# Kernel optimization log

Hardware: AMD Instinct MI355X
Metric: run time of the kernel (lower is better)

Reference implementation:

```python
import jax, jax.numpy as jnp
import numpy as np

N = 500_000
E = 16_000_000


def setup_inputs() -> dict:
    key = jax.random.key(0)
    k1, k2, k3, k4, k5 = jax.random.split(key, 5)
    x = jax.random.uniform(k1, (N, 11), dtype=jnp.float32)
    edge_index = jax.random.randint(k2, (2, E), 0, N, dtype=jnp.int32)
    edge_weight = jax.random.uniform(k3, (E,), dtype=jnp.float32)
    W1 = jax.random.normal(k4, (11, 16), dtype=jnp.float32) * 0.3
    b1 = jnp.zeros((16,), jnp.float32)
    W2 = jax.random.normal(k5, (16, 2), dtype=jnp.float32) * 0.3
    b2 = jnp.zeros((2,), jnp.float32)
    return {"x": x, "edge_index": edge_index, "edge_weight": edge_weight,
            "W1": W1, "b1": b1, "W2": W2, "b2": b2}


def gcn_norm(edge_index, edge_weight, n):
    # GCNConv(normalize=True, add_self_loops=True): A_hat = D^-1/2 (A + I) D^-1/2
    self_idx = jnp.arange(n, dtype=edge_index.dtype)
    row = jnp.concatenate([edge_index[0], self_idx])  # source
    col = jnp.concatenate([edge_index[1], self_idx])  # target
    w = jnp.concatenate([edge_weight, jnp.ones((n,), edge_weight.dtype)])
    deg = jax.ops.segment_sum(w, col, num_segments=n)
    dinv = jnp.where(deg > 0, jax.lax.rsqrt(deg), 0.0)
    norm = dinv[row] * w * dinv[col]
    return row, col, norm


def gcn_conv(x, row, col, norm, W, b, n):
    h = x @ W                                   # [N, F_out]
    msg = norm[:, None] * h[row]                # gather + scale, [E+N, F_out]
    out = jax.ops.segment_sum(msg, col, num_segments=n)  # scatter-add
    return out + b


def reference(x, edge_index, edge_weight, W1, b1, W2, b2):
    n = x.shape[0]
    row, col, norm = gcn_norm(edge_index, edge_weight, n)
    h = jax.nn.relu(gcn_conv(x, row, col, norm, W1, b1, n))
    # dropout is identity in eval / deterministic reference
    h = gcn_conv(h, row, col, norm, W2, b2, n)
    return jax.nn.log_softmax(h, axis=1)
```

## Files before the change

kernel.cpp:

```cpp
#include <hip/hip_runtime.h>
#include <math.h>


typedef unsigned long long u64;
typedef unsigned int u32;
typedef _Float16 f16;
typedef __attribute__((ext_vector_type(4))) _Float16 f16x4;

#define BKT    512
#define NBMAX  1024
#define NBLK   256


__global__ __launch_bounds__(256) void k_count(const int* __restrict__ col,
                                               u32* __restrict__ hist_g,
                                               int NB, int E, int CH) {
    __shared__ u32 cnt[NBMAX];
    for (int b = threadIdx.x; b < NB; b += 256) cnt[b] = 0;
    __syncthreads();
    int blk = blockIdx.x;
    int s = blk * CH, e = min(s + CH, E);
    for (int i = s + threadIdx.x; i < e; i += 256) {
        int c = __builtin_nontemporal_load(col + i);
        atomicAdd(&cnt[c >> 9], 1u);
    }
    __syncthreads();
    for (int b = threadIdx.x; b < NB; b += 256)
        hist_g[(size_t)blk * NB + b] = cnt[b];
}

__global__ __launch_bounds__(256) void k_colsum(const u32* __restrict__ hist_g,
                                                u32* __restrict__ colsum, int NB) {
    int k = blockIdx.x * 256 + threadIdx.x;
    if (k >= NB) return;
    u32 s = 0;
    for (int j = 0; j < NBLK; j++) s += hist_g[(size_t)j * NB + k];
    colsum[k] = s;
}

__global__ __launch_bounds__(256) void k_scan_sums32(u32* __restrict__ bsum, int nb) {
    __shared__ u32 s[256];
    __shared__ u32 carry;
    int t = threadIdx.x;
    if (t == 0) carry = 0;
    __syncthreads();
    int chunks = (nb + 255) / 256;
    for (int ch = 0; ch < chunks; ch++) {
        int i = ch * 256 + t;
        u32 v = (i < nb) ? bsum[i] : 0;
        s[t] = v;
        __syncthreads();
        for (int off = 1; off < 256; off <<= 1) {
            u32 u = (t >= off) ? s[t - off] : 0;
            __syncthreads();
            s[t] += u;
            __syncthreads();
        }
        u32 incl = s[t];
        u32 my_carry = carry;
        if (i < nb) bsum[i] = incl - v + my_carry;
        __syncthreads();
        if (t == 0) carry = my_carry + s[255];
        __syncthreads();
    }
}

__global__ __launch_bounds__(256) void k_basefill(const u32* __restrict__ hist_g,
                                                  const u32* __restrict__ keybase,
                                                  u32* __restrict__ base_g, int NB) {
    int k = blockIdx.x * 256 + threadIdx.x;
    if (k >= NB) return;
    u32 run = keybase[k];
    for (int j = 0; j < NBLK; j++) {
        base_g[(size_t)j * NB + k] = run;
        run += hist_g[(size_t)j * NB + k];
    }
}

__global__ __launch_bounds__(256) void k_scatter(const int* __restrict__ row,
                                                 const int* __restrict__ col,
                                                 const float* __restrict__ w,
                                                 const u32* __restrict__ base_g,
                                                 u64* __restrict__ edge_g,
                                                 int NB, int E, int CH) {
    __shared__ u32 cursor[NBMAX];
    int blk = blockIdx.x;
    for (int b = threadIdx.x; b < NB; b += 256)
        cursor[b] = base_g[(size_t)blk * NB + b];
    __syncthreads();
    int s = blk * CH, e = min(s + CH, E);
    for (int i = s + threadIdx.x; i < e; i += 256) {
        int c = __builtin_nontemporal_load(col + i);
        int r = __builtin_nontemporal_load(row + i);
        float wv = __builtin_nontemporal_load(w + i);
        int b = c >> 9;
        u32 pos = atomicAdd(&cursor[b], 1u);
        u64 rec = ((u64)__float_as_uint(wv) << 32)
                | ((u64)(u32)(c & 511) << 19) | (u64)(u32)r;
        edge_g[pos] = rec;
    }
}


__global__ __launch_bounds__(256) void k_prep(const u64* __restrict__ edge_g,
                                              const u32* __restrict__ kb,
                                              const float* __restrict__ x,
                                              float* __restrict__ dinv_g,
                                              f16* __restrict__ xs0,
                                              f16* __restrict__ xs1,
                                              f16* __restrict__ xs2,
                                              int NB, int n, int E) {
    __shared__ float degw[BKT];
    int b = blockIdx.x;
    for (int j = threadIdx.x; j < BKT; j += 256) degw[j] = 1.0f;
    __syncthreads();
    int s = (int)kb[b];
    int e = (b + 1 < NB) ? (int)kb[b + 1] : E;
    for (int i = s + threadIdx.x; i < e; i += 256) {
        u64 rec = __builtin_nontemporal_load(edge_g + i);
        int cl = (int)(((u32)rec >> 19) & 511u);
        float wv = __uint_as_float((u32)(rec >> 32));
        atomicAdd(&degw[cl], wv);
    }
    __syncthreads();
    int node0 = b << 9;
    int nn = min(BKT, n - node0);
    for (int j = threadIdx.x; j < nn; j += 256) {
        int node = node0 + j;
        float dv = rsqrtf(degw[j]);
        dinv_g[node] = dv;
        const float* xp = x + (size_t)node * 11;
        f16x4 a, bq, c;
#pragma unroll
        for (int k = 0; k < 4; k++) a[k]  = (f16)(dv * xp[k]);
#pragma unroll
        for (int k = 0; k < 4; k++) bq[k] = (f16)(dv * xp[4 + k]);
        c[0] = (f16)(dv * xp[8]);
        c[1] = (f16)(dv * xp[9]);
        c[2] = (f16)(dv * xp[10]);
        c[3] = (f16)0.f;
        *(f16x4*)(xs0 + ((size_t)node << 2)) = a;
        *(f16x4*)(xs1 + ((size_t)node << 2)) = bq;
        *(f16x4*)(xs2 + ((size_t)node << 2)) = c;
    }
}


__global__ __launch_bounds__(512) void k_csrsort(const u64* __restrict__ edge_g,
                                                 const u32* __restrict__ kb,
                                                 u64* __restrict__ edge2_g,
                                                 u32* __restrict__ runstart,
                                                 int NB, int n, int E) {
    __shared__ u32 cnt[BKT];
    __shared__ u32 off[BKT];
    __shared__ u32 cur[BKT];
    int t = threadIdx.x;
    int b = blockIdx.x;
    int node0 = b << 9;
    int s = (int)kb[b];
    int e = (b + 1 < NB) ? (int)kb[b + 1] : E;
    cnt[t] = 0;
    __syncthreads();
    for (int i = s + t; i < e; i += 512) {
        u32 lo = (u32)edge_g[i];
        atomicAdd(&cnt[(lo >> 19) & 511u], 1u);
    }
    __syncthreads();
    off[t] = cnt[t];
    __syncthreads();
    for (int d = 1; d < 512; d <<= 1) {
        u32 v = (t >= d) ? off[t - d] : 0;
        __syncthreads();
        off[t] += v;
        __syncthreads();
    }
    u32 mystart = (u32)s + off[t] - cnt[t];
    cur[t] = mystart;
    runstart[node0 + t] = mystart;
    if (t == 511) runstart[node0 + 512] = (u32)e;
    __syncthreads();
    for (int i = s + t; i < e; i += 512) {
        u64 rec = edge_g[i];
        int cl = (int)(((u32)rec >> 19) & 511u);
        u32 pos = atomicAdd(&cur[cl], 1u);
        edge2_g[pos] = rec;
    }
}


__global__ __launch_bounds__(256) void k_pass(const u64* __restrict__ edge2_g,
                                              const u32* __restrict__ runstart,
                                              const f16* __restrict__ xsp,
                                              float4* __restrict__ aggp, int n) {
    int node = blockIdx.x * 256 + threadIdx.x;
    if (node >= n) return;
    f16x4 selfv = *(const f16x4*)(xsp + ((size_t)node << 2));
    float a0 = (float)selfv[0], a1 = (float)selfv[1];
    float a2 = (float)selfv[2], a3 = (float)selfv[3];
    int p = (int)runstart[node], pe = (int)runstart[node + 1];
    for (; p + 3 < pe; p += 4) {
        u64 r0 = __builtin_nontemporal_load(edge2_g + p);
        u64 r1 = __builtin_nontemporal_load(edge2_g + p + 1);
        u64 r2 = __builtin_nontemporal_load(edge2_g + p + 2);
        u64 r3 = __builtin_nontemporal_load(edge2_g + p + 3);
        f16x4 g0 = *(const f16x4*)(xsp + ((size_t)((u32)r0 & 0x7FFFFu) << 2));
        f16x4 g1 = *(const f16x4*)(xsp + ((size_t)((u32)r1 & 0x7FFFFu) << 2));
        f16x4 g2 = *(const f16x4*)(xsp + ((size_t)((u32)r2 & 0x7FFFFu) << 2));
        f16x4 g3 = *(const f16x4*)(xsp + ((size_t)((u32)r3 & 0x7FFFFu) << 2));
        float w0 = __uint_as_float((u32)(r0 >> 32));
        float w1 = __uint_as_float((u32)(r1 >> 32));
        float w2 = __uint_as_float((u32)(r2 >> 32));
        float w3 = __uint_as_float((u32)(r3 >> 32));
        a0 += w0 * (float)g0[0] + w1 * (float)g1[0] + w2 * (float)g2[0] + w3 * (float)g3[0];
        a1 += w0 * (float)g0[1] + w1 * (float)g1[1] + w2 * (float)g2[1] + w3 * (float)g3[1];
        a2 += w0 * (float)g0[2] + w1 * (float)g1[2] + w2 * (float)g2[2] + w3 * (float)g3[2];
        a3 += w0 * (float)g0[3] + w1 * (float)g1[3] + w2 * (float)g2[3] + w3 * (float)g3[3];
    }
    for (; p < pe; p++) {
        u64 r0 = edge2_g[p];
        f16x4 g0 = *(const f16x4*)(xsp + ((size_t)((u32)r0 & 0x7FFFFu) << 2));
        float w0 = __uint_as_float((u32)(r0 >> 32));
        a0 += w0 * (float)g0[0];
        a1 += w0 * (float)g0[1];
        a2 += w0 * (float)g0[2];
        a3 += w0 * (float)g0[3];
    }
    float4 ov; ov.x = a0; ov.y = a1; ov.z = a2; ov.w = a3;
    aggp[node] = ov;
}


__global__ __launch_bounds__(256) void k_mlp(const float4* __restrict__ agg0,
                                             const float4* __restrict__ agg1,
                                             const float4* __restrict__ agg2,
                                             const float* __restrict__ dinv_g,
                                             const float* __restrict__ W1,
                                             const float* __restrict__ b1,
                                             const float* __restrict__ W2,
                                             float* __restrict__ h2s, int n) {
    __shared__ float sW1[176];
    __shared__ float sb1[16];
    __shared__ float sW2[32];
    for (int t = threadIdx.x; t < 176; t += 256) sW1[t] = W1[t];
    if (threadIdx.x < 16) sb1[threadIdx.x] = b1[threadIdx.x];
    if (threadIdx.x >= 64 && threadIdx.x < 96) sW2[threadIdx.x - 64] = W2[threadIdx.x - 64];
    __syncthreads();
    int node = blockIdx.x * 256 + threadIdx.x;
    if (node >= n) return;
    float dv = dinv_g[node];
    float4 v0 = agg0[node], v1 = agg1[node], v2 = agg2[node];
    float v[11];
    v[0] = dv * v0.x; v[1] = dv * v0.y; v[2]  = dv * v0.z; v[3] = dv * v0.w;
    v[4] = dv * v1.x; v[5] = dv * v1.y; v[6]  = dv * v1.z; v[7] = dv * v1.w;
    v[8] = dv * v2.x; v[9] = dv * v2.y; v[10] = dv * v2.z;
    float o0 = 0.f, o1 = 0.f;
#pragma unroll
    for (int f = 0; f < 16; f++) {
        float hh = sb1[f];
#pragma unroll
        for (int k = 0; k < 11; k++) hh += v[k] * sW1[k * 16 + f];
        hh = fmaxf(hh, 0.f);
        o0 += hh * sW2[f * 2 + 0];
        o1 += hh * sW2[f * 2 + 1];
    }
    float2 ov; ov.x = dv * o0; ov.y = dv * o1;
    *(float2*)(h2s + ((size_t)node << 1)) = ov;
}


__global__ __launch_bounds__(256) void k_pull2_csr(const u64* __restrict__ edge2_g,
                                                   const u32* __restrict__ runstart,
                                                   const float* __restrict__ h2s,
                                                   const float* __restrict__ dinv_g,
                                                   const float* __restrict__ b2,
                                                   float* __restrict__ out, int n) {
    int node = blockIdx.x * 256 + threadIdx.x;
    if (node >= n) return;
    float2 selfv = *(const float2*)(h2s + (size_t)node * 2);
    float a0 = selfv.x, a1 = selfv.y;
    int p = (int)runstart[node], pe = (int)runstart[node + 1];
    for (; p + 3 < pe; p += 4) {
        u64 r0 = __builtin_nontemporal_load(edge2_g + p);
        u64 r1 = __builtin_nontemporal_load(edge2_g + p + 1);
        u64 r2 = __builtin_nontemporal_load(edge2_g + p + 2);
        u64 r3 = __builtin_nontemporal_load(edge2_g + p + 3);
        float2 g0 = *(const float2*)(h2s + (size_t)((u32)r0 & 0x7FFFFu) * 2);
        float2 g1 = *(const float2*)(h2s + (size_t)((u32)r1 & 0x7FFFFu) * 2);
        float2 g2 = *(const float2*)(h2s + (size_t)((u32)r2 & 0x7FFFFu) * 2);
        float2 g3 = *(const float2*)(h2s + (size_t)((u32)r3 & 0x7FFFFu) * 2);
        float w0 = __uint_as_float((u32)(r0 >> 32));
        float w1 = __uint_as_float((u32)(r1 >> 32));
        float w2 = __uint_as_float((u32)(r2 >> 32));
        float w3 = __uint_as_float((u32)(r3 >> 32));
        a0 += w0 * g0.x + w1 * g1.x + w2 * g2.x + w3 * g3.x;
        a1 += w0 * g0.y + w1 * g1.y + w2 * g2.y + w3 * g3.y;
    }
    for (; p < pe; p++) {
        u64 r0 = edge2_g[p];
        float2 g0 = *(const float2*)(h2s + (size_t)((u32)r0 & 0x7FFFFu) * 2);
        float w0 = __uint_as_float((u32)(r0 >> 32));
        a0 += w0 * g0.x;
        a1 += w0 * g0.y;
    }
    float dv = dinv_g[node];
    float v0 = dv * a0 + b2[0];
    float v1 = dv * a1 + b2[1];
    float m = fmaxf(v0, v1);
    float lse = m + logf(expf(v0 - m) + expf(v1 - m));
    float2 ov; ov.x = v0 - lse; ov.y = v1 - lse;
    *(float2*)(out + (size_t)node * 2) = ov;
}


__global__ __launch_bounds__(256) void k_init_deg(float* deg, int n) {
    int i = blockIdx.x * blockDim.x + threadIdx.x;
    if (i < n) deg[i] = 1.0f;
}

__global__ __launch_bounds__(256) void k_deg_accum(const int* __restrict__ col,
                                                   const float* __restrict__ w,
                                                   float* __restrict__ deg, int E) {
    int i = blockIdx.x * blockDim.x + threadIdx.x;
    if (i < E) atomicAdd(&deg[col[i]], w[i]);
}

__global__ __launch_bounds__(256) void k_rsqrt(float* deg, int n) {
    int i = blockIdx.x * blockDim.x + threadIdx.x;
    if (i < n) {
        float d = deg[i];
        deg[i] = (d > 0.0f) ? rsqrtf(d) : 0.0f;
    }
}

__global__ __launch_bounds__(256) void k_gemm1_plain(const float* __restrict__ x,
                                                     const float* __restrict__ W1,
                                                     float* __restrict__ h1, int n) {
    __shared__ float sW[176];
    for (int t = threadIdx.x; t < 176; t += blockDim.x) sW[t] = W1[t];
    __syncthreads();
    int i = blockIdx.x * blockDim.x + threadIdx.x;
    if (i >= n) return;
    float xi[11];
#pragma unroll
    for (int k = 0; k < 11; k++) xi[k] = x[(size_t)i * 11 + k];
#pragma unroll
    for (int f = 0; f < 16; f++) {
        float acc = 0.0f;
#pragma unroll
        for (int k = 0; k < 11; k++) acc += xi[k] * sW[k * 16 + f];
        h1[(size_t)i * 16 + f] = acc;
    }
}

__global__ __launch_bounds__(256) void k_scatter16(const int* __restrict__ row,
                                                   const int* __restrict__ col,
                                                   const float* __restrict__ w,
                                                   const float* __restrict__ dinv,
                                                   const float* __restrict__ h1,
                                                   float* __restrict__ acc, int E) {
    int i = blockIdx.x * blockDim.x + threadIdx.x;
    if (i >= E) return;
    int r = row[i], c = col[i];
    float nw = dinv[r] * w[i] * dinv[c];
    const float4* hr = (const float4*)(h1 + (size_t)r * 16);
    float* o = acc + (size_t)c * 16;
#pragma unroll
    for (int q = 0; q < 4; q++) {
        float4 hv = hr[q];
        atomicAdd(o + q * 4 + 0, nw * hv.x);
        atomicAdd(o + q * 4 + 1, nw * hv.y);
        atomicAdd(o + q * 4 + 2, nw * hv.z);
        atomicAdd(o + q * 4 + 3, nw * hv.w);
    }
}

__global__ __launch_bounds__(256) void k_post1(const float* __restrict__ h1,
                                               const float* __restrict__ dinv,
                                               const float* __restrict__ b1,
                                               float* __restrict__ acc, int n) {
    int i = blockIdx.x * blockDim.x + threadIdx.x;
    if (i >= n) return;
    float dv = dinv[i];
    float cs = dv * dv;
#pragma unroll
    for (int f = 0; f < 16; f++) {
        float v = acc[(size_t)i * 16 + f] + cs * h1[(size_t)i * 16 + f] + b1[f];
        acc[(size_t)i * 16 + f] = v > 0.0f ? v : 0.0f;
    }
}

__global__ __launch_bounds__(256) void k_gemm2(const float* __restrict__ hrelu,
                                               const float* __restrict__ W2,
                                               float* __restrict__ h2, int n) {
    __shared__ float sW[32];
    for (int t = threadIdx.x; t < 32; t += blockDim.x) sW[t] = W2[t];
    __syncthreads();
    int i = blockIdx.x * blockDim.x + threadIdx.x;
    if (i >= n) return;
    float a0 = 0.0f, a1 = 0.0f;
#pragma unroll
    for (int f = 0; f < 16; f++) {
        float h = hrelu[(size_t)i * 16 + f];
        a0 += h * sW[f * 2 + 0];
        a1 += h * sW[f * 2 + 1];
    }
    h2[(size_t)i * 2 + 0] = a0;
    h2[(size_t)i * 2 + 1] = a1;
}

__global__ __launch_bounds__(256) void k_scatter2(const int* __restrict__ row,
                                                  const int* __restrict__ col,
                                                  const float* __restrict__ w,
                                                  const float* __restrict__ dinv,
                                                  const float* __restrict__ h2,
                                                  float* __restrict__ out, int E) {
    int i = blockIdx.x * blockDim.x + threadIdx.x;
    if (i >= E) return;
    int r = row[i], c = col[i];
    float nw = dinv[r] * w[i] * dinv[c];
    atomicAdd(&out[(size_t)c * 2 + 0], nw * h2[(size_t)r * 2 + 0]);
    atomicAdd(&out[(size_t)c * 2 + 1], nw * h2[(size_t)r * 2 + 1]);
}

__global__ __launch_bounds__(256) void k_final(const float* __restrict__ h2,
                                               const float* __restrict__ dinv,
                                               const float* __restrict__ b2,
                                               float* __restrict__ out, int n) {
    int i = blockIdx.x * blockDim.x + threadIdx.x;
    if (i >= n) return;
    float dv = dinv[i];
    float cs = dv * dv;
    float v0 = out[(size_t)i * 2 + 0] + cs * h2[(size_t)i * 2 + 0] + b2[0];
    float v1 = out[(size_t)i * 2 + 1] + cs * h2[(size_t)i * 2 + 1] + b2[1];
    float m = fmaxf(v0, v1);
    float lse = m + logf(expf(v0 - m) + expf(v1 - m));
    out[(size_t)i * 2 + 0] = v0 - lse;
    out[(size_t)i * 2 + 1] = v1 - lse;
}


static inline size_t align64(size_t x) { return (x + 63) & ~(size_t)63; }

extern "C" void kernel_launch(void* const* d_in, const int* in_sizes, int n_in,
                              void* d_out, int out_size, void* d_ws, size_t ws_size,
                              hipStream_t stream) {
    const float* x  = (const float*)d_in[0];
    const int*   ei = (const int*)d_in[1];
    const float* ew = (const float*)d_in[2];
    const float* W1 = (const float*)d_in[3];
    const float* b1 = (const float*)d_in[4];
    const float* W2 = (const float*)d_in[5];
    const float* b2 = (const float*)d_in[6];

    const int n = in_sizes[0] / 11;
    const int E = in_sizes[2];
    const int* rowp = ei;
    const int* colp = ei + E;

    const int TB = 256;
    const int gN = (n + TB - 1) / TB;
    const int gE = (E + TB - 1) / TB;

    const int NB = (n + BKT - 1) / BKT;
    const int CH = (E + NBLK - 1) / NBLK;

    float* outf = (float*)d_out;

    char* base = (char*)d_ws;
    size_t M = (size_t)NBLK * NB;
    size_t o_hist = 0;
    size_t o_base = align64(o_hist + M * 4);
    size_t o_kb   = align64(o_base + M * 4);
    size_t o_dinv = align64(o_kb + (size_t)(NB + 2) * 4);
    size_t o_xs0  = align64(o_dinv + (size_t)n * 4);
    size_t o_xs1  = align64(o_xs0 + (size_t)n * 8);
    size_t o_xs2  = align64(o_xs1 + (size_t)n * 8);
    size_t o_ag0  = align64(o_xs2 + (size_t)n * 8);
    size_t o_ag1  = align64(o_ag0 + (size_t)n * 16);
    size_t o_ag2  = align64(o_ag1 + (size_t)n * 16);
    size_t o_h2   = align64(o_ag2 + (size_t)n * 16);
    size_t o_run  = align64(o_h2 + (size_t)n * 2 * 4);
    size_t o_edge = align64(o_run + (size_t)(n + BKT + 2) * 4);
    size_t o_edge2 = align64(o_edge + (size_t)E * 8);
    size_t needed = align64(o_edge2 + (size_t)E * 8);

    if (ws_size >= needed && n <= (1 << 19) && NB <= NBMAX) {
        u32*    hist_g = (u32*)(base + o_hist);
        u32*    base_g = (u32*)(base + o_base);
        u32*    kb     = (u32*)(base + o_kb);
        float*  dinv_g = (float*)(base + o_dinv);
        f16*    xs0    = (f16*)(base + o_xs0);
        f16*    xs1    = (f16*)(base + o_xs1);
        f16*    xs2    = (f16*)(base + o_xs2);
        float4* agg0   = (float4*)(base + o_ag0);
        float4* agg1   = (float4*)(base + o_ag1);
        float4* agg2   = (float4*)(base + o_ag2);
        float*  h2s    = (float*)(base + o_h2);
        u32*    runst  = (u32*)(base + o_run);
        u64*    edge_g = (u64*)(base + o_edge);
        u64*    edge2_g = (u64*)(base + o_edge2);

        const int KBg = (NB + 255) / 256;

        k_count<<<NBLK, TB, 0, stream>>>(colp, hist_g, NB, E, CH);
        k_colsum<<<KBg, TB, 0, stream>>>(hist_g, kb, NB);
        k_scan_sums32<<<1, TB, 0, stream>>>(kb, NB);
        k_basefill<<<KBg, TB, 0, stream>>>(hist_g, kb, base_g, NB);
        k_scatter<<<NBLK, TB, 0, stream>>>(rowp, colp, ew, base_g, edge_g, NB, E, CH);
        k_prep<<<NB, TB, 0, stream>>>(edge_g, kb, x, dinv_g, xs0, xs1, xs2, NB, n, E);
        k_csrsort<<<NB, 512, 0, stream>>>(edge_g, kb, edge2_g, runst, NB, n, E);
        k_pass<<<gN, TB, 0, stream>>>(edge2_g, runst, xs0, agg0, n);
        k_pass<<<gN, TB, 0, stream>>>(edge2_g, runst, xs1, agg1, n);
        k_pass<<<gN, TB, 0, stream>>>(edge2_g, runst, xs2, agg2, n);
        k_mlp<<<gN, TB, 0, stream>>>(agg0, agg1, agg2, dinv_g, W1, b1, W2, h2s, n);
        k_pull2_csr<<<gN, TB, 0, stream>>>(edge2_g, runst, h2s, dinv_g, b2, outf, n);
    } else {
        float* ws   = (float*)d_ws;
        float* dinv = ws;
        float* h1   = ws + (size_t)n;
        float* acc1 = ws + (size_t)n * 17;

        k_init_deg<<<gN, TB, 0, stream>>>(dinv, n);
        k_deg_accum<<<gE, TB, 0, stream>>>(colp, ew, dinv, E);
        k_rsqrt<<<gN, TB, 0, stream>>>(dinv, n);

        k_gemm1_plain<<<gN, TB, 0, stream>>>(x, W1, h1, n);
        hipMemsetAsync(acc1, 0, (size_t)n * 16 * sizeof(float), stream);
        k_scatter16<<<gE, TB, 0, stream>>>(rowp, colp, ew, dinv, h1, acc1, E);
        k_post1<<<gN, TB, 0, stream>>>(h1, dinv, b1, acc1, n);

        float* h2 = h1;
        k_gemm2<<<gN, TB, 0, stream>>>(acc1, W2, h2, n);
        hipMemsetAsync(outf, 0, (size_t)n * 2 * sizeof(float), stream);
        k_scatter2<<<gE, TB, 0, stream>>>(rowp, colp, ew, dinv, h2, outf, E);
        k_final<<<gN, TB, 0, stream>>>(h2, dinv, b2, outf, n);
    }
}
```

Measured before the change: 1.682 ms.

## Stage scatter writes in LDS by bucket and fold degree into CSR sort

Both the bucket scatter and the per-bucket CSR sort now process edges in 4096-edge chunks. Each chunk is locally counting-sorted in shared memory, so global writes land in contiguous runs per bucket instead of randomly scattered 8-byte stores. The degree accumulation moves from k_prep into the first pass of k_csrsort, which removes one full read of the edge array, and k_prep becomes a simple per-node kernel. NBLK doubles and blocks use 512 threads. In exchange, each block uses much more LDS and adds extra scans and barriers per chunk.

```diff
diff --git a/kernel.cpp b/kernel.cpp
--- a/kernel.cpp
+++ b/kernel.cpp
@@ -4,12 +4,14 @@
 
 typedef unsigned long long u64;
 typedef unsigned int u32;
+typedef unsigned short u16;
 typedef _Float16 f16;
 typedef __attribute__((ext_vector_type(4))) _Float16 f16x4;
 
 #define BKT    512
 #define NBMAX  1024
-#define NBLK   256
+#define NBLK   512
+#define CHUNK  4096
 
 
 __global__ __launch_bounds__(256) void k_count(const int* __restrict__ col,
@@ -77,71 +79,74 @@
     }
 }
 
-__global__ __launch_bounds__(256) void k_scatter(const int* __restrict__ row,
+
+__global__ __launch_bounds__(512) void k_scatter(const int* __restrict__ row,
                                                  const int* __restrict__ col,
                                                  const float* __restrict__ w,
                                                  const u32* __restrict__ base_g,
                                                  u64* __restrict__ edge_g,
                                                  int NB, int E, int CH) {
+    __shared__ u64 stage[CHUNK];
+    __shared__ u16 skey[CHUNK];
     __shared__ u32 cursor[NBMAX];
+    __shared__ u32 ccnt[NBMAX];
+    __shared__ u32 cbase[NBMAX];
+    __shared__ u32 sscan[512];
+    int t = threadIdx.x;
     int blk = blockIdx.x;
-    for (int b = threadIdx.x; b < NB; b += 256)
-        cursor[b] = base_g[(size_t)blk * NB + b];
-    __syncthreads();
+    for (int b = t; b < NB; b += 512) cursor[b] = base_g[(size_t)blk * NB + b];
     int s = blk * CH, e = min(s + CH, E);
-    for (int i = s + threadIdx.x; i < e; i += 256) {
-        int c = __builtin_nontemporal_load(col + i);
-        int r = __builtin_nontemporal_load(row + i);
-        float wv = __builtin_nontemporal_load(w + i);
-        int b = c >> 9;
-        u32 pos = atomicAdd(&cursor[b], 1u);
-        u64 rec = ((u64)__float_as_uint(wv) << 32)
-                | ((u64)(u32)(c & 511) << 19) | (u64)(u32)r;
-        edge_g[pos] = rec;
-    }
-}
-
-
-__global__ __launch_bounds__(256) void k_prep(const u64* __restrict__ edge_g,
-                                              const u32* __restrict__ kb,
-                                              const float* __restrict__ x,
-                                              float* __restrict__ dinv_g,
-                                              f16* __restrict__ xs0,
-                                              f16* __restrict__ xs1,
-                                              f16* __restrict__ xs2,
-                                              int NB, int n, int E) {
-    __shared__ float degw[BKT];
-    int b = blockIdx.x;
-    for (int j = threadIdx.x; j < BKT; j += 256) degw[j] = 1.0f;
-    __syncthreads();
-    int s = (int)kb[b];
-    int e = (b + 1 < NB) ? (int)kb[b + 1] : E;
-    for (int i = s + threadIdx.x; i < e; i += 256) {
-        u64 rec = __builtin_nontemporal_load(edge_g + i);
-        int cl = (int)(((u32)rec >> 19) & 511u);
-        float wv = __uint_as_float((u32)(rec >> 32));
-        atomicAdd(&degw[cl], wv);
-    }
-    __syncthreads();
-    int node0 = b << 9;
-    int nn = min(BKT, n - node0);
-    for (int j = threadIdx.x; j < nn; j += 256) {
-        int node = node0 + j;
-        float dv = rsqrtf(degw[j]);
-        dinv_g[node] = dv;
-        const float* xp = x + (size_t)node * 11;
-        f16x4 a, bq, c;
-#pragma unroll
-        for (int k = 0; k < 4; k++) a[k]  = (f16)(dv * xp[k]);
-#pragma unroll
-        for (int k = 0; k < 4; k++) bq[k] = (f16)(dv * xp[4 + k]);
-        c[0] = (f16)(dv * xp[8]);
-        c[1] = (f16)(dv * xp[9]);
-        c[2] = (f16)(dv * xp[10]);
-        c[3] = (f16)0.f;
-        *(f16x4*)(xs0 + ((size_t)node << 2)) = a;
-        *(f16x4*)(xs1 + ((size_t)node << 2)) = bq;
-        *(f16x4*)(xs2 + ((size_t)node << 2)) = c;
+    for (int c0 = s; c0 < e; c0 += CHUNK) {
+        int cend = min(c0 + CHUNK, e);
+        for (int b = t; b < NB; b += 512) ccnt[b] = 0;
+        __syncthreads();
+        u64 rec[8]; u32 rnk[8]; int key[8];
+#pragma unroll
+        for (int q = 0; q < 8; q++) {
+            int i = c0 + q * 512 + t;
+            if (i < cend) {
+                int c  = __builtin_nontemporal_load(col + i);
+                int r  = __builtin_nontemporal_load(row + i);
+                float wv = __builtin_nontemporal_load(w + i);
+                int k = c >> 9;
+                rec[q] = ((u64)__float_as_uint(wv) << 32)
+                       | ((u64)(u32)(c & 511) << 19) | (u64)(u32)r;
+                key[q] = k;
+                rnk[q] = atomicAdd(&ccnt[k], 1u);
+            } else key[q] = -1;
+        }
+        __syncthreads();
+        u32 a0 = (2 * t     < NB) ? ccnt[2 * t]     : 0;
+        u32 a1 = (2 * t + 1 < NB) ? ccnt[2 * t + 1] : 0;
+        sscan[t] = a0 + a1;
+        __syncthreads();
+        for (int d = 1; d < 512; d <<= 1) {
+            u32 v = (t >= d) ? sscan[t - d] : 0;
+            __syncthreads();
+            sscan[t] += v;
+            __syncthreads();
+        }
+        u32 bse = (t > 0) ? sscan[t - 1] : 0;
+        if (2 * t     < NB) cbase[2 * t]     = bse;
+        if (2 * t + 1 < NB) cbase[2 * t + 1] = bse + a0;
+        __syncthreads();
+#pragma unroll
+        for (int q = 0; q < 8; q++) {
+            if (key[q] >= 0) {
+                u32 slot = cbase[key[q]] + rnk[q];
+                stage[slot] = rec[q];
+                skey[slot] = (u16)key[q];
+            }
+        }
+        __syncthreads();
+        int tot = cend - c0;
+        for (int j = t; j < tot; j += 512) {
+            int k = skey[j];
+            edge_g[cursor[k] + (u32)j - cbase[k]] = stage[j];
+        }
+        __syncthreads();
+        for (int b = t; b < NB; b += 512) cursor[b] += ccnt[b];
+        __syncthreads();
     }
 }
 
@@ -150,41 +155,115 @@
                                                  const u32* __restrict__ kb,
                                                  u64* __restrict__ edge2_g,
                                                  u32* __restrict__ runstart,
+                                                 float* __restrict__ dinv_g,
                                                  int NB, int n, int E) {
+    __shared__ u64 stage[CHUNK];
+    __shared__ u16 skey[CHUNK];
     __shared__ u32 cnt[BKT];
-    __shared__ u32 off[BKT];
+    __shared__ float sdeg[BKT];
     __shared__ u32 cur[BKT];
+    __shared__ u32 ccnt[BKT];
+    __shared__ u32 cbase[BKT];
     int t = threadIdx.x;
     int b = blockIdx.x;
     int node0 = b << 9;
     int s = (int)kb[b];
     int e = (b + 1 < NB) ? (int)kb[b + 1] : E;
     cnt[t] = 0;
+    sdeg[t] = 1.0f;
     __syncthreads();
     for (int i = s + t; i < e; i += 512) {
-        u32 lo = (u32)edge_g[i];
-        atomicAdd(&cnt[(lo >> 19) & 511u], 1u);
-    }
-    __syncthreads();
-    off[t] = cnt[t];
+        u64 rec = __builtin_nontemporal_load(edge_g + i);
+        int cl = (int)(((u32)rec >> 19) & 511u);
+        atomicAdd(&cnt[cl], 1u);
+        atomicAdd(&sdeg[cl], __uint_as_float((u32)(rec >> 32)));
+    }
+    __syncthreads();
+    ccnt[t] = cnt[t];
     __syncthreads();
     for (int d = 1; d < 512; d <<= 1) {
-        u32 v = (t >= d) ? off[t - d] : 0;
-        __syncthreads();
-        off[t] += v;
-        __syncthreads();
-    }
-    u32 mystart = (u32)s + off[t] - cnt[t];
+        u32 v = (t >= d) ? ccnt[t - d] : 0;
+        __syncthreads();
+        ccnt[t] += v;
+        __syncthreads();
+    }
+    u32 mystart = (u32)s + ccnt[t] - cnt[t];
     cur[t] = mystart;
     runstart[node0 + t] = mystart;
     if (t == 511) runstart[node0 + 512] = (u32)e;
-    __syncthreads();
-    for (int i = s + t; i < e; i += 512) {
-        u64 rec = edge_g[i];
-        int cl = (int)(((u32)rec >> 19) & 511u);
-        u32 pos = atomicAdd(&cur[cl], 1u);
-        edge2_g[pos] = rec;
-    }
+    if (node0 + t < n) dinv_g[node0 + t] = rsqrtf(sdeg[t]);
+    __syncthreads();
+    for (int c0 = s; c0 < e; c0 += CHUNK) {
+        int cend = min(c0 + CHUNK, e);
+        ccnt[t] = 0;
+        __syncthreads();
+        u64 rec[8]; u32 rnk[8]; int key[8];
+#pragma unroll
+        for (int q = 0; q < 8; q++) {
+            int i = c0 + q * 512 + t;
+            if (i < cend) {
+                u64 r = __builtin_nontemporal_load(edge_g + i);
+                int cl = (int)(((u32)r >> 19) & 511u);
+                rec[q] = r;
+                key[q] = cl;
+                rnk[q] = atomicAdd(&ccnt[cl], 1u);
+            } else key[q] = -1;
+        }
+        __syncthreads();
+        cbase[t] = ccnt[t];
+        __syncthreads();
+        for (int d = 1; d < 512; d <<= 1) {
+            u32 v = (t >= d) ? cbase[t - d] : 0;
+            __syncthreads();
+            cbase[t] += v;
+            __syncthreads();
+        }
+        u32 myexc = cbase[t] - ccnt[t];
+        __syncthreads();
+        cbase[t] = myexc;
+        __syncthreads();
+#pragma unroll
+        for (int q = 0; q < 8; q++) {
+            if (key[q] >= 0) {
+                u32 slot = cbase[key[q]] + rnk[q];
+                stage[slot] = rec[q];
+                skey[slot] = (u16)key[q];
+            }
+        }
+        __syncthreads();
+        int tot = cend - c0;
+        for (int j = t; j < tot; j += 512) {
+            int k = skey[j];
+            edge2_g[cur[k] + (u32)j - cbase[k]] = stage[j];
+        }
+        __syncthreads();
+        cur[t] += ccnt[t];
+        __syncthreads();
+    }
+}
+
+
+__global__ __launch_bounds__(256) void k_prep(const float* __restrict__ x,
+                                              const float* __restrict__ dinv_g,
+                                              f16* __restrict__ xs0,
+                                              f16* __restrict__ xs1,
+                                              f16* __restrict__ xs2, int n) {
+    int node = blockIdx.x * 256 + threadIdx.x;
+    if (node >= n) return;
+    float dv = dinv_g[node];
+    const float* xp = x + (size_t)node * 11;
+    f16x4 a, bq, c;
+#pragma unroll
+    for (int k = 0; k < 4; k++) a[k]  = (f16)(dv * xp[k]);
+#pragma unroll
+    for (int k = 0; k < 4; k++) bq[k] = (f16)(dv * xp[4 + k]);
+    c[0] = (f16)(dv * xp[8]);
+    c[1] = (f16)(dv * xp[9]);
+    c[2] = (f16)(dv * xp[10]);
+    c[3] = (f16)0.f;
+    *(f16x4*)(xs0 + ((size_t)node << 2)) = a;
+    *(f16x4*)(xs1 + ((size_t)node << 2)) = bq;
+    *(f16x4*)(xs2 + ((size_t)node << 2)) = c;
 }
 
 
@@ -506,9 +585,9 @@
         k_colsum<<<KBg, TB, 0, stream>>>(hist_g, kb, NB);
         k_scan_sums32<<<1, TB, 0, stream>>>(kb, NB);
         k_basefill<<<KBg, TB, 0, stream>>>(hist_g, kb, base_g, NB);
-        k_scatter<<<NBLK, TB, 0, stream>>>(rowp, colp, ew, base_g, edge_g, NB, E, CH);
-        k_prep<<<NB, TB, 0, stream>>>(edge_g, kb, x, dinv_g, xs0, xs1, xs2, NB, n, E);
-        k_csrsort<<<NB, 512, 0, stream>>>(edge_g, kb, edge2_g, runst, NB, n, E);
+        k_scatter<<<NBLK, 512, 0, stream>>>(rowp, colp, ew, base_g, edge_g, NB, E, CH);
+        k_csrsort<<<NB, 512, 0, stream>>>(edge_g, kb, edge2_g, runst, dinv_g, NB, n, E);
+        k_prep<<<gN, TB, 0, stream>>>(x, dinv_g, xs0, xs1, xs2, n);
         k_pass<<<gN, TB, 0, stream>>>(edge2_g, runst, xs0, agg0, n);
         k_pass<<<gN, TB, 0, stream>>>(edge2_g, runst, xs1, agg1, n);
         k_pass<<<gN, TB, 0, stream>>>(edge2_g, runst, xs2, agg2, n);
```

Result: faster. 1.432 ms (-14.8%).
